# Kernel optimization log

Measured on AMD Instinct MI355X. Metric: run time of the kernel, lower is better.

The kernel has to match this reference:

```python
import jax, jax.numpy as jnp
import numpy as np

D_MODEL = 1024
HEADS = 16
D_K = D_MODEL // HEADS


def setup_inputs() -> dict:
    key = jax.random.key(0)
    ks = jax.random.split(key, 11)
    bs, seq = 2, 2048
    scale = 1.0 / np.sqrt(D_MODEL)
    inp = {
        "query": jax.random.normal(ks[0], (bs, seq, D_MODEL), jnp.float32),
        "key": jax.random.normal(ks[1], (bs, seq, D_MODEL), jnp.float32),
        "value": jax.random.normal(ks[2], (bs, seq, D_MODEL), jnp.float32),
        # nn.Linear weights: y = x @ W.T + b, W shape [out, in]
        "Wq": jax.random.normal(ks[3], (D_MODEL, D_MODEL), jnp.float32) * scale,
        "bq": jnp.zeros((D_MODEL,), jnp.float32),
        "Wk": jax.random.normal(ks[4], (D_MODEL, D_MODEL), jnp.float32) * scale,
        "bk": jnp.zeros((D_MODEL,), jnp.float32),
        "Wv": jax.random.normal(ks[5], (D_MODEL, D_MODEL), jnp.float32) * scale,
        "bv": jnp.zeros((D_MODEL,), jnp.float32),
        "Wo": jax.random.normal(ks[6], (D_MODEL, D_MODEL), jnp.float32) * scale,
        "bo": jnp.zeros((D_MODEL,), jnp.float32),
    }
    return inp


def _split_heads(x, bs):
    # [b, s, d_model] -> [b, h, s, d_k]
    return x.reshape(bs, -1, HEADS, D_K).transpose(0, 2, 1, 3)


def reference(query, key, value, Wq, bq, Wk, bk, Wv, bv, Wo, bo):
    bs = query.shape[0]
    q = _split_heads(query @ Wq.T + bq, bs)
    k = _split_heads(key @ Wk.T + bk, bs)
    v = _split_heads(value @ Wv.T + bv, bs)
    # scaled dot-product attention (dropout is identity at eval)
    logits = jnp.einsum("bhqd,bhkd->bhqk", q, k) / np.sqrt(D_K).astype(np.float32)
    probs = jax.nn.softmax(logits, axis=-1)
    scores = jnp.einsum("bhqk,bhkd->bhqd", probs, v)  # [b, h, s, d_k]
    concat = scores.transpose(0, 2, 1, 3).reshape(bs, -1, D_MODEL)
    output = concat @ Wo.T + bo
    return (output, scores)
```

## Files before the change

### kernel.cpp

```cpp
#include <hip/hip_runtime.h>
#include <stdint.h>
#include <math.h>

typedef __bf16 bf16;
typedef __bf16 bf16x4 __attribute__((ext_vector_type(4)));
typedef __bf16 bf16x8 __attribute__((ext_vector_type(8)));
typedef float floatx4 __attribute__((ext_vector_type(4)));

#define CEXP 0.1803368801111204f

__global__ __launch_bounds__(256) void wcvt_kernel(
    const float* __restrict__ Wq, const float* __restrict__ Wk,
    const float* __restrict__ Wv, const float* __restrict__ Wo,
    bf16* __restrict__ dst)
{
  const float* src = (blockIdx.y == 0) ? Wq : (blockIdx.y == 1) ? Wk
                   : (blockIdx.y == 2) ? Wv : Wo;
  bf16* d = dst + (size_t)blockIdx.y * 1048576;
  const int i = (blockIdx.x * 256 + threadIdx.x) * 4;
  const floatx4 v = *(const floatx4*)(src + i);
  bf16x4 o;
#pragma unroll
  for (int j = 0; j < 4; ++j) o[j] = (bf16)v[j];
  *(bf16x4*)(d + i) = o;
}

__device__ __forceinline__ void gemm_body(
    const float* __restrict__ A, const bf16* __restrict__ Ab,
    const bf16* __restrict__ Wb, const float* __restrict__ bias,
    void* __restrict__ Cout, const int mode, const float oscale)
{
  __shared__ __align__(16) bf16 As[128 * 72];
  __shared__ __align__(16) bf16 Bs[128 * 72];
  const int tid  = threadIdx.x;
  const int wave = tid >> 6;
  const int lane = tid & 63;
  const int mlane = lane & 15;
  const int quad  = lane >> 4;
  const int m0 = blockIdx.x * 128;
  const int n0 = blockIdx.y * 128;
  const int wm = (wave >> 1) * 64;
  const int wn = (wave & 1) * 64;
  const int arow = tid >> 4, ac4 = (tid & 15) * 4;
  const int wrow = tid >> 3, wc8 = (tid & 7) * 8;

  floatx4 a_pf[8];
  bf16x8  ab_pf[4];
  bf16x8  w_pf[4];

  auto load_a = [&](int k0) {
    if (mode == 1) {
#pragma unroll
      for (int c = 0; c < 4; ++c) {
        const int token = m0 + c * 32 + wrow;
        const int b = token >> 11, s = token & 2047;
        const int h = k0 >> 6;
        ab_pf[c] = *(const bf16x8*)(Ab + (((size_t)(b * 16 + h) * 2048 + s) << 6) + wc8);
      }
    } else {
#pragma unroll
      for (int rr = 0; rr < 8; ++rr)
        a_pf[rr] = *(const floatx4*)(A + (size_t)(m0 + rr * 16 + arow) * 1024 + k0 + ac4);
    }
  };
  auto load_w = [&](int k0) {
#pragma unroll
    for (int c = 0; c < 4; ++c)
      w_pf[c] = *(const bf16x8*)(Wb + (size_t)(n0 + c * 32 + wrow) * 1024 + k0 + wc8);
  };

  load_a(0);
  load_w(0);

  floatx4 acc[4][4] = {};

  for (int k0 = 0; k0 < 1024; k0 += 64) {
    if (mode == 1) {
#pragma unroll
      for (int c = 0; c < 4; ++c)
        *(bf16x8*)&As[(c * 32 + wrow) * 72 + wc8] = ab_pf[c];
    } else {
#pragma unroll
      for (int rr = 0; rr < 8; ++rr) {
        bf16x4 ac;
#pragma unroll
        for (int j = 0; j < 4; ++j) ac[j] = (bf16)a_pf[rr][j];
        *(bf16x4*)&As[(rr * 16 + arow) * 72 + ac4] = ac;
      }
    }
#pragma unroll
    for (int c = 0; c < 4; ++c)
      *(bf16x8*)&Bs[(c * 32 + wrow) * 72 + wc8] = w_pf[c];
    __syncthreads();

    if (k0 + 64 < 1024) { load_a(k0 + 64); load_w(k0 + 64); }

#pragma unroll
    for (int kk = 0; kk < 64; kk += 32) {
      bf16x8 af[4], bfr[4];
#pragma unroll
      for (int t = 0; t < 4; ++t) {
        af[t]  = *(const bf16x8*)&As[(wm + t * 16 + mlane) * 72 + kk + quad * 8];
        bfr[t] = *(const bf16x8*)&Bs[(wn + t * 16 + mlane) * 72 + kk + quad * 8];
      }
#pragma unroll
      for (int mt = 0; mt < 4; ++mt)
#pragma unroll
        for (int nt = 0; nt < 4; ++nt)
          acc[mt][nt] = __builtin_amdgcn_mfma_f32_16x16x32_bf16(
              af[mt], bfr[nt], acc[mt][nt], 0, 0, 0);
    }
    __syncthreads();
  }

#pragma unroll
  for (int nt = 0; nt < 4; ++nt) {
    const int col = n0 + wn + nt * 16 + mlane;
    const float bv = bias[col];
#pragma unroll
    for (int mt = 0; mt < 4; ++mt) {
#pragma unroll
      for (int r = 0; r < 4; ++r) {
        const int row = m0 + wm + mt * 16 + quad * 4 + r;
        const float v = (acc[mt][nt][r] + bv) * oscale;
        if (mode == 0) {
          const int b = row >> 11, s = row & 2047;
          const int h = col >> 6, dk = col & 63;
          ((bf16*)Cout)[(((size_t)(b * 16 + h) * 2048 + s) << 6) + dk] = (bf16)v;
        } else if (mode == 2) {
          const int b = row >> 11, s = row & 2047;
          const int h = col >> 6, dk = col & 63;
          ((bf16*)Cout)[(((size_t)(b * 16 + h) * 64 + dk) << 11) + s] = (bf16)v;
        } else {
          ((float*)Cout)[(size_t)row * 1024 + col] = v;
        }
      }
    }
  }
}

__global__ __launch_bounds__(256) void qkv_kernel(
    const float* __restrict__ q, const float* __restrict__ k, const float* __restrict__ v,
    const bf16* __restrict__ Wb,
    const float* __restrict__ bq, const float* __restrict__ bk, const float* __restrict__ bv,
    bf16* __restrict__ Qw, bf16* __restrict__ Kw, bf16* __restrict__ Vw)
{
  const int z = blockIdx.z;
  const float* A = (z == 0) ? q : (z == 1) ? k : v;
  const bf16* W  = Wb + (size_t)z * 1048576;
  const float* B = (z == 0) ? bq : (z == 1) ? bk : bv;
  if (z == 2)      gemm_body(A, nullptr, W, B, Vw, 2, 1.0f);
  else if (z == 1) gemm_body(A, nullptr, W, B, Kw, 0, 1.0f);
  else             gemm_body(A, nullptr, W, B, Qw, 0, CEXP);
}

__global__ __launch_bounds__(256) void out_kernel(
    const bf16* __restrict__ Sb, const bf16* __restrict__ Wob,
    const float* __restrict__ bo, float* __restrict__ out)
{
  gemm_body(nullptr, Sb, Wob, bo, out, 1, 1.0f);
}

__global__ __launch_bounds__(256) void attn_kernel(
    const bf16* __restrict__ Qw, const bf16* __restrict__ Kw,
    const bf16* __restrict__ Vtg, float* __restrict__ scores,
    bf16* __restrict__ Sb)
{
  __shared__ __align__(16) bf16 Ks[64 * 72];
  __shared__ __align__(16) bf16 Vt[64 * 72];
  __shared__ __align__(16) bf16 Ps[4][32 * 72];

  const int tid  = threadIdx.x;
  const int wave = tid >> 6;
  const int lane = tid & 63;
  const int mlane = lane & 15;
  const int quad  = lane >> 4;
  const int bh = blockIdx.y;
  const int q0 = blockIdx.x * 128;
  const size_t base = (size_t)bh << 17;

  const int srow = tid >> 3, sc8 = (tid & 7) * 8;

  bf16x8 qf[2][2];
#pragma unroll
  for (int qt = 0; qt < 2; ++qt)
#pragma unroll
    for (int c = 0; c < 2; ++c)
      qf[qt][c] = *(const bf16x8*)
          &Qw[base + (size_t)(q0 + wave * 32 + qt * 16 + mlane) * 64 + c * 32 + quad * 8];

  float rs[2] = {0.f, 0.f};
  floatx4 o[2][4] = {};

  bf16x8 kpf[2], vpf[2];
  auto load_kv = [&](int kt) {
#pragma unroll
    for (int rr = 0; rr < 2; ++rr) {
      const int row = rr * 32 + srow;
      kpf[rr] = *(const bf16x8*)&Kw[base + (size_t)(kt + row) * 64 + sc8];
      vpf[rr] = *(const bf16x8*)&Vtg[base + (size_t)row * 2048 + kt + sc8];
    }
  };
  load_kv(0);

  for (int kt = 0; kt < 2048; kt += 64) {
    __syncthreads();
#pragma unroll
    for (int rr = 0; rr < 2; ++rr) {
      const int row = rr * 32 + srow;
      *(bf16x8*)&Ks[row * 72 + sc8] = kpf[rr];
      *(bf16x8*)&Vt[row * 72 + sc8] = vpf[rr];
    }
    __syncthreads();
    if (kt + 64 < 2048) load_kv(kt + 64);

#pragma unroll
    for (int nt = 0; nt < 4; ++nt) {
      bf16x8 a0 = *(const bf16x8*)&Ks[(nt * 16 + mlane) * 72 + quad * 8];
      bf16x8 a1 = *(const bf16x8*)&Ks[(nt * 16 + mlane) * 72 + 32 + quad * 8];
      floatx4 s0 = {}, s1 = {};
      s0 = __builtin_amdgcn_mfma_f32_16x16x32_bf16(a0, qf[0][0], s0, 0, 0, 0);
      s0 = __builtin_amdgcn_mfma_f32_16x16x32_bf16(a1, qf[0][1], s0, 0, 0, 0);
      s1 = __builtin_amdgcn_mfma_f32_16x16x32_bf16(a0, qf[1][0], s1, 0, 0, 0);
      s1 = __builtin_amdgcn_mfma_f32_16x16x32_bf16(a1, qf[1][1], s1, 0, 0, 0);

      bf16x4 pk0, pk1;
#pragma unroll
      for (int r = 0; r < 4; ++r) {
        const float p0 = exp2f(s0[r]);
        const float p1 = exp2f(s1[r]);
        rs[0] += p0; rs[1] += p1;
        pk0[r] = (bf16)p0; pk1[r] = (bf16)p1;
      }
      *(bf16x4*)&Ps[wave][(mlane)      * 72 + nt * 16 + quad * 4] = pk0;
      *(bf16x4*)&Ps[wave][(16 + mlane) * 72 + nt * 16 + quad * 4] = pk1;
    }

    asm volatile("s_waitcnt lgkmcnt(0)" ::: "memory");

#pragma unroll
    for (int c = 0; c < 2; ++c) {
      bf16x8 pa0 = *(const bf16x8*)&Ps[wave][(mlane)      * 72 + c * 32 + quad * 8];
      bf16x8 pa1 = *(const bf16x8*)&Ps[wave][(16 + mlane) * 72 + c * 32 + quad * 8];
#pragma unroll
      for (int nt = 0; nt < 4; ++nt) {
        bf16x8 vb = *(const bf16x8*)&Vt[(nt * 16 + mlane) * 72 + c * 32 + quad * 8];
        o[0][nt] = __builtin_amdgcn_mfma_f32_16x16x32_bf16(pa0, vb, o[0][nt], 0, 0, 0);
        o[1][nt] = __builtin_amdgcn_mfma_f32_16x16x32_bf16(pa1, vb, o[1][nt], 0, 0, 0);
      }
    }
  }

#pragma unroll
  for (int qt = 0; qt < 2; ++qt) {
    rs[qt] += __shfl_xor(rs[qt], 16, 64);
    rs[qt] += __shfl_xor(rs[qt], 32, 64);
  }
  const float inv0 = 1.0f / rs[0];
  const float inv1 = 1.0f / rs[1];

#pragma unroll
  for (int qt = 0; qt < 2; ++qt) {
#pragma unroll
    for (int r = 0; r < 4; ++r) {
      const float invr = __shfl(qt ? inv1 : inv0, quad * 4 + r, 64);
      const int row = q0 + wave * 32 + qt * 16 + quad * 4 + r;
#pragma unroll
      for (int nt = 0; nt < 4; ++nt) {
        const float val = o[qt][nt][r] * invr;
        const size_t idx = base + (size_t)row * 64 + nt * 16 + mlane;
        scores[idx] = val;
        Sb[idx] = (bf16)val;
      }
    }
  }
}

extern "C" void kernel_launch(void* const* d_in, const int* in_sizes, int n_in,
                              void* d_out, int out_size, void* d_ws, size_t ws_size,
                              hipStream_t stream) {
  const float* query = (const float*)d_in[0];
  const float* key   = (const float*)d_in[1];
  const float* value = (const float*)d_in[2];
  const float* Wq = (const float*)d_in[3];
  const float* bq = (const float*)d_in[4];
  const float* Wk = (const float*)d_in[5];
  const float* bk = (const float*)d_in[6];
  const float* Wv = (const float*)d_in[7];
  const float* bv = (const float*)d_in[8];
  const float* Wo = (const float*)d_in[9];
  const float* bo = (const float*)d_in[10];

  float* out    = (float*)d_out;
  float* scores = out + (size_t)4194304;

  bf16* Wb  = (bf16*)d_ws;
  bf16* Qws = Wb + (size_t)4194304;
  bf16* Kws = Qws + (size_t)4194304;
  bf16* Vws = Kws + (size_t)4194304;
  bf16* Sb  = Vws + (size_t)4194304;

  wcvt_kernel<<<dim3(1024, 4), 256, 0, stream>>>(Wq, Wk, Wv, Wo, Wb);
  qkv_kernel<<<dim3(32, 8, 3), 256, 0, stream>>>(query, key, value, Wb,
                                                 bq, bk, bv, Qws, Kws, Vws);
  attn_kernel<<<dim3(16, 32), 256, 0, stream>>>(Qws, Kws, Vws, scores, Sb);
  out_kernel<<<dim3(32, 8), 256, 0, stream>>>(Sb, Wb + (size_t)3145728, bo, out);
}
```

Before: 246.7 us.

## Stage transposed V store in LDS and halve attention query tile per block

The V projection epilogue now writes its transposed output through shared memory, so global stores become contiguous 16-byte vectors instead of scattered 2-byte writes. The attention kernel drops from 128 to 64 query rows per block and doubles the grid, using a remapped block index to spread heads across the GPU. The softmax row sum is now computed with an MFMA against a ones vector instead of scalar adds and shuffles, and MFMA sections get raised wave priority. Each block now reloads K/V for fewer queries, which roughly doubles K/V traffic from L2, in exchange for more parallelism and fewer registers per wave.

```diff
diff --git a/kernel.cpp b/kernel.cpp
--- a/kernel.cpp
+++ b/kernel.cpp
@@ -113,6 +113,37 @@
     __syncthreads();
   }
 
+  if (mode == 2) {
+    bf16* T = (wave < 2) ? &As[wave * 4608] : &Bs[(wave - 2) * 4608];
+#pragma unroll
+    for (int nt = 0; nt < 4; ++nt) {
+      const float bv = bias[n0 + wn + nt * 16 + mlane];
+#pragma unroll
+      for (int mt = 0; mt < 4; ++mt) {
+        bf16x4 t4;
+#pragma unroll
+        for (int r = 0; r < 4; ++r)
+          t4[r] = (bf16)((acc[mt][nt][r] + bv) * oscale);
+        *(bf16x4*)&T[(nt * 16 + mlane) * 72 + mt * 16 + quad * 4] = t4;
+      }
+    }
+    asm volatile("s_waitcnt lgkmcnt(0)" ::: "memory");
+    const int token0 = m0 + wm;
+    const int bb = token0 >> 11;
+    const int srow0 = token0 & 2047;
+    const int h = (n0 + wn) >> 6;
+    const int dl = lane >> 3;
+    const int s8 = (lane & 7) * 8;
+    bf16* outp = (bf16*)Cout + ((size_t)(bb * 16 + h) << 17);
+#pragma unroll
+    for (int p = 0; p < 8; ++p) {
+      const int dk = p * 8 + dl;
+      const bf16x8 v8 = *(const bf16x8*)&T[dk * 72 + s8];
+      *(bf16x8*)&outp[((size_t)dk << 11) + srow0 + s8] = v8;
+    }
+    return;
+  }
+
 #pragma unroll
   for (int nt = 0; nt < 4; ++nt) {
     const int col = n0 + wn + nt * 16 + mlane;
@@ -127,10 +158,6 @@
           const int b = row >> 11, s = row & 2047;
           const int h = col >> 6, dk = col & 63;
           ((bf16*)Cout)[(((size_t)(b * 16 + h) * 2048 + s) << 6) + dk] = (bf16)v;
-        } else if (mode == 2) {
-          const int b = row >> 11, s = row & 2047;
-          const int h = col >> 6, dk = col & 63;
-          ((bf16*)Cout)[(((size_t)(b * 16 + h) * 64 + dk) << 11) + s] = (bf16)v;
         } else {
           ((float*)Cout)[(size_t)row * 1024 + col] = v;
         }
@@ -168,29 +195,34 @@
 {
   __shared__ __align__(16) bf16 Ks[64 * 72];
   __shared__ __align__(16) bf16 Vt[64 * 72];
-  __shared__ __align__(16) bf16 Ps[4][32 * 72];
+  __shared__ __align__(16) bf16 Ps[4][16 * 72];
 
   const int tid  = threadIdx.x;
   const int wave = tid >> 6;
   const int lane = tid & 63;
   const int mlane = lane & 15;
   const int quad  = lane >> 4;
-  const int bh = blockIdx.y;
-  const int q0 = blockIdx.x * 128;
+
+  const int g = blockIdx.x + (blockIdx.y << 5);
+  const int slot = g >> 3;
+  const int bh = ((g & 7) << 2) + (slot >> 5);
+  const int q0 = (slot & 31) << 6;
   const size_t base = (size_t)bh << 17;
 
   const int srow = tid >> 3, sc8 = (tid & 7) * 8;
 
-  bf16x8 qf[2][2];
-#pragma unroll
-  for (int qt = 0; qt < 2; ++qt)
-#pragma unroll
-    for (int c = 0; c < 2; ++c)
-      qf[qt][c] = *(const bf16x8*)
-          &Qw[base + (size_t)(q0 + wave * 32 + qt * 16 + mlane) * 64 + c * 32 + quad * 8];
-
-  float rs[2] = {0.f, 0.f};
-  floatx4 o[2][4] = {};
+  bf16x8 qf[2];
+#pragma unroll
+  for (int c = 0; c < 2; ++c)
+    qf[c] = *(const bf16x8*)
+        &Qw[base + (size_t)(q0 + wave * 16 + mlane) * 64 + c * 32 + quad * 8];
+
+  bf16x8 ones;
+#pragma unroll
+  for (int j = 0; j < 8; ++j) ones[j] = (bf16)1.0f;
+
+  floatx4 o[4] = {};
+  floatx4 osum = {};
 
   bf16x8 kpf[2], vpf[2];
   auto load_kv = [&](int kt) {
@@ -218,60 +250,44 @@
     for (int nt = 0; nt < 4; ++nt) {
       bf16x8 a0 = *(const bf16x8*)&Ks[(nt * 16 + mlane) * 72 + quad * 8];
       bf16x8 a1 = *(const bf16x8*)&Ks[(nt * 16 + mlane) * 72 + 32 + quad * 8];
-      floatx4 s0 = {}, s1 = {};
-      s0 = __builtin_amdgcn_mfma_f32_16x16x32_bf16(a0, qf[0][0], s0, 0, 0, 0);
-      s0 = __builtin_amdgcn_mfma_f32_16x16x32_bf16(a1, qf[0][1], s0, 0, 0, 0);
-      s1 = __builtin_amdgcn_mfma_f32_16x16x32_bf16(a0, qf[1][0], s1, 0, 0, 0);
-      s1 = __builtin_amdgcn_mfma_f32_16x16x32_bf16(a1, qf[1][1], s1, 0, 0, 0);
-
-      bf16x4 pk0, pk1;
-#pragma unroll
-      for (int r = 0; r < 4; ++r) {
-        const float p0 = exp2f(s0[r]);
-        const float p1 = exp2f(s1[r]);
-        rs[0] += p0; rs[1] += p1;
-        pk0[r] = (bf16)p0; pk1[r] = (bf16)p1;
-      }
-      *(bf16x4*)&Ps[wave][(mlane)      * 72 + nt * 16 + quad * 4] = pk0;
-      *(bf16x4*)&Ps[wave][(16 + mlane) * 72 + nt * 16 + quad * 4] = pk1;
+      floatx4 s0 = {};
+      __builtin_amdgcn_s_setprio(1);
+      s0 = __builtin_amdgcn_mfma_f32_16x16x32_bf16(a0, qf[0], s0, 0, 0, 0);
+      s0 = __builtin_amdgcn_mfma_f32_16x16x32_bf16(a1, qf[1], s0, 0, 0, 0);
+      __builtin_amdgcn_s_setprio(0);
+      bf16x4 pk;
+#pragma unroll
+      for (int r = 0; r < 4; ++r) pk[r] = (bf16)exp2f(s0[r]);
+      *(bf16x4*)&Ps[wave][mlane * 72 + nt * 16 + quad * 4] = pk;
     }
 
     asm volatile("s_waitcnt lgkmcnt(0)" ::: "memory");
 
-#pragma unroll
-    for (int c = 0; c < 2; ++c) {
-      bf16x8 pa0 = *(const bf16x8*)&Ps[wave][(mlane)      * 72 + c * 32 + quad * 8];
-      bf16x8 pa1 = *(const bf16x8*)&Ps[wave][(16 + mlane) * 72 + c * 32 + quad * 8];
-#pragma unroll
-      for (int nt = 0; nt < 4; ++nt) {
-        bf16x8 vb = *(const bf16x8*)&Vt[(nt * 16 + mlane) * 72 + c * 32 + quad * 8];
-        o[0][nt] = __builtin_amdgcn_mfma_f32_16x16x32_bf16(pa0, vb, o[0][nt], 0, 0, 0);
-        o[1][nt] = __builtin_amdgcn_mfma_f32_16x16x32_bf16(pa1, vb, o[1][nt], 0, 0, 0);
-      }
-    }
-  }
-
-#pragma unroll
-  for (int qt = 0; qt < 2; ++qt) {
-    rs[qt] += __shfl_xor(rs[qt], 16, 64);
-    rs[qt] += __shfl_xor(rs[qt], 32, 64);
-  }
-  const float inv0 = 1.0f / rs[0];
-  const float inv1 = 1.0f / rs[1];
-
-#pragma unroll
-  for (int qt = 0; qt < 2; ++qt) {
-#pragma unroll
-    for (int r = 0; r < 4; ++r) {
-      const float invr = __shfl(qt ? inv1 : inv0, quad * 4 + r, 64);
-      const int row = q0 + wave * 32 + qt * 16 + quad * 4 + r;
-#pragma unroll
-      for (int nt = 0; nt < 4; ++nt) {
-        const float val = o[qt][nt][r] * invr;
-        const size_t idx = base + (size_t)row * 64 + nt * 16 + mlane;
-        scores[idx] = val;
-        Sb[idx] = (bf16)val;
-      }
+    bf16x8 pa0 = *(const bf16x8*)&Ps[wave][mlane * 72 + quad * 8];
+    bf16x8 pa1 = *(const bf16x8*)&Ps[wave][mlane * 72 + 32 + quad * 8];
+    __builtin_amdgcn_s_setprio(1);
+    osum = __builtin_amdgcn_mfma_f32_16x16x32_bf16(pa0, ones, osum, 0, 0, 0);
+    osum = __builtin_amdgcn_mfma_f32_16x16x32_bf16(pa1, ones, osum, 0, 0, 0);
+#pragma unroll
+    for (int nt = 0; nt < 4; ++nt) {
+      bf16x8 vb0 = *(const bf16x8*)&Vt[(nt * 16 + mlane) * 72 + quad * 8];
+      bf16x8 vb1 = *(const bf16x8*)&Vt[(nt * 16 + mlane) * 72 + 32 + quad * 8];
+      o[nt] = __builtin_amdgcn_mfma_f32_16x16x32_bf16(pa0, vb0, o[nt], 0, 0, 0);
+      o[nt] = __builtin_amdgcn_mfma_f32_16x16x32_bf16(pa1, vb1, o[nt], 0, 0, 0);
+    }
+    __builtin_amdgcn_s_setprio(0);
+  }
+
+#pragma unroll
+  for (int r = 0; r < 4; ++r) {
+    const float inv = 1.0f / osum[r];
+    const int row = q0 + wave * 16 + quad * 4 + r;
+#pragma unroll
+    for (int nt = 0; nt < 4; ++nt) {
+      const float val = o[nt][r] * inv;
+      const size_t idx = base + (size_t)row * 64 + nt * 16 + mlane;
+      scores[idx] = val;
+      Sb[idx] = (bf16)val;
     }
   }
 }
@@ -303,6 +319,6 @@
   wcvt_kernel<<<dim3(1024, 4), 256, 0, stream>>>(Wq, Wk, Wv, Wo, Wb);
   qkv_kernel<<<dim3(32, 8, 3), 256, 0, stream>>>(query, key, value, Wb,
                                                  bq, bk, bv, Qws, Kws, Vws);
-  attn_kernel<<<dim3(16, 32), 256, 0, stream>>>(Qws, Kws, Vws, scores, Sb);
+  attn_kernel<<<dim3(32, 32), 256, 0, stream>>>(Qws, Kws, Vws, scores, Sb);
   out_kernel<<<dim3(32, 8), 256, 0, stream>>>(Sb, Wb + (size_t)3145728, bo, out);
 }
```

Result: no change. 242.9 us (-1.6%).
